# Kernel tuning notes

Hardware: AMD Instinct MI355X
Metric: run time of the kernel (lower is better)

Reference implementation:

```python
import jax, jax.numpy as jnp
import numpy as np

NF = 64
DG = 8
NB = 5
K = 3
K2 = K * K


def conv2d(x, w, b):
    # x: [B,C,H,W], w: [O,I,3,3] -> SAME padding, stride 1
    y = jax.lax.conv_general_dilated(x, w, (1, 1), 'SAME',
                                     dimension_numbers=('NCHW', 'OIHW', 'NCHW'))
    return y + b[None, :, None, None]


def dcn(x, off_feat, cw, cb, w, b):
    """Modulated deformable conv (DCNv2, extra_offset_mask=True).
    x: [B,C,H,W] sampled input; off_feat: [B,C,H,W] feeds conv_offset_mask.
    cw/cb: offset-mask conv params [3*DG*K2, C, 3, 3]; w/b: main conv [O, C, 3, 3].
    """
    B, C, H, W = x.shape
    Cg = C // DG
    om = conv2d(off_feat, cw, cb)                      # [B, 3*DG*K2, H, W]
    o1, o2, m = jnp.split(om, 3, axis=1)
    dy = o1.reshape(B, DG, K2, H, W)
    dx = o2.reshape(B, DG, K2, H, W)
    mask = jax.nn.sigmoid(m).reshape(B, DG, K2, H, W)
    # kernel tap offsets for 3x3, pad=1, dilation=1
    kyy, kxx = np.meshgrid(np.arange(K) - 1, np.arange(K) - 1, indexing='ij')
    ky = jnp.asarray(kyy.reshape(K2), x.dtype)
    kx = jnp.asarray(kxx.reshape(K2), x.dtype)
    gy = jnp.arange(H, dtype=x.dtype)
    gx = jnp.arange(W, dtype=x.dtype)
    py = gy[None, None, None, :, None] + ky[None, None, :, None, None] + dy  # [B,DG,K2,H,W]
    px = gx[None, None, None, None, :] + kx[None, None, :, None, None] + dx
    y0 = jnp.floor(py)
    x0 = jnp.floor(px)
    wy = py - y0
    wx = px - x0
    y0i = y0.astype(jnp.int32)
    x0i = x0.astype(jnp.int32)
    xg = x.reshape(B, DG, Cg, H * W)

    def gather(iy, ix):
        valid = ((iy >= 0) & (iy < H) & (ix >= 0) & (ix < W)).astype(x.dtype)
        lin = (jnp.clip(iy, 0, H - 1) * W + jnp.clip(ix, 0, W - 1)).reshape(B, DG, 1, K2 * H * W)
        v = jnp.take_along_axis(xg, jnp.broadcast_to(lin, (B, DG, Cg, K2 * H * W)), axis=3)
        return v.reshape(B, DG, Cg, K2, H, W) * valid[:, :, None]

    v00 = gather(y0i, x0i)
    v01 = gather(y0i, x0i + 1)
    v10 = gather(y0i + 1, x0i)
    v11 = gather(y0i + 1, x0i + 1)
    wy_ = wy[:, :, None]
    wx_ = wx[:, :, None]
    val = (v00 * (1 - wy_) * (1 - wx_) + v01 * (1 - wy_) * wx_
           + v10 * wy_ * (1 - wx_) + v11 * wy_ * wx_) * mask[:, :, None]  # [B,DG,Cg,K2,H,W]
    wr = w.reshape(w.shape[0], DG, Cg, K2)
    out = jnp.einsum('bgckhw,ogck->bohw', val, wr) + b[None, :, None, None]
    return out


def setup_inputs() -> dict:
    key = jax.random.key(0)
    ks = jax.random.split(key, 16)

    def w_(k, shape, s=0.05):
        return jax.random.normal(k, shape, jnp.float32) * s

    B, N, C, H, W = 4, 5, 1, 128, 128
    inp = {}
    inp['x'] = jax.random.normal(ks[0], (B, N, C, H, W), jnp.float32)
    inp['w_init'] = w_(ks[1], (NF, C, 3, 3))
    inp['b_init'] = jnp.zeros((NF,), jnp.float32)
    inp['res_w1'] = w_(ks[2], (NB, NF, NF, 3, 3))
    inp['res_b1'] = jnp.zeros((NB, NF), jnp.float32)
    inp['res_w2'] = w_(ks[3], (NB, NF, NF, 3, 3))
    inp['res_b2'] = jnp.zeros((NB, NF), jnp.float32)
    inp['w_bn'] = w_(ks[4], (NF, 2 * NF, 3, 3))
    inp['b_bn'] = jnp.zeros((NF,), jnp.float32)
    inp['off_w'] = w_(ks[5], (4, NF, NF, 3, 3))
    inp['off_b'] = jnp.zeros((4, NF), jnp.float32)
    inp['com_w'] = w_(ks[6], (4, 3 * DG * K2, NF, 3, 3), 0.01)
    inp['com_b'] = jnp.zeros((4, 3 * DG * K2), jnp.float32)
    inp['dcn_w'] = w_(ks[7], (4, NF, NF, 3, 3))
    inp['dcn_b'] = jnp.zeros((4, NF), jnp.float32)
    inp['w_rec'] = w_(ks[8], (C, NF, 3, 3))
    inp['b_rec'] = jnp.zeros((C,), jnp.float32)
    return inp


def reference(x, w_init, b_init, res_w1, res_b1, res_w2, res_b2, w_bn, b_bn,
              off_w, off_b, com_w, com_b, dcn_w, dcn_b, w_rec, b_rec):
    B, N, C, H, W = x.shape
    y = x.reshape(B * N, C, H, W)
    out = jax.nn.relu(conv2d(y, w_init, b_init))
    for i in range(NB):  # ResidualBlock_noBN x nb
        h = jax.nn.relu(conv2d(out, res_w1[i], res_b1[i]))
        out = out + conv2d(h, res_w2[i], res_b2[i])
    out = out.reshape(B, N, NF, H, W)
    ref = out[:, N // 2]
    ys = []
    for i in range(N):
        nei = out[:, i]
        fea = conv2d(jnp.concatenate([ref, nei], axis=1), w_bn, b_bn)
        o = conv2d(fea, off_w[0], off_b[0])
        fea = dcn(fea, o, com_w[0], com_b[0], dcn_w[0], dcn_b[0])
        o = conv2d(fea, off_w[1], off_b[1])
        fea = dcn(fea, o, com_w[1], com_b[1], dcn_w[1], dcn_b[1])
        o = conv2d(fea, off_w[2], off_b[2])
        fea = dcn(nei, o, com_w[2], com_b[2], dcn_w[2], dcn_b[2])
        o = conv2d(fea, off_w[3], off_b[3])
        aligned = dcn(fea, o, com_w[3], com_b[3], dcn_w[3], dcn_b[3])
        ys.append(conv2d(aligned, w_rec, b_rec))
    return jnp.concatenate(ys, axis=1)  # [B, N*C, H, W]
```

## Files before the change

### kernel.cpp

```cpp
#include <hip/hip_runtime.h>
#include <hip/hip_bf16.h>

typedef __hip_bfloat16 bf16;
typedef __attribute__((ext_vector_type(8))) short short8;
typedef __attribute__((ext_vector_type(4))) float floatx4;
typedef unsigned short ush;

#define HH 128
#define WW 128
#define HW 16384

__device__ __forceinline__ float b2f(bf16 v){ return __bfloat162float(v); }
__device__ __forceinline__ float bfu2f(ush u){
  union{unsigned int i; float f;} c; c.i = ((unsigned int)u)<<16; return c.f;
}
__device__ __forceinline__ ush f2bfu(float f){
  bf16 h = __float2bfloat16(f);
  return *(ush*)&h;
}

__global__ void detect_dtype(const ush* __restrict__ x, float* __restrict__ flag){
  __shared__ int bad;
  if (threadIdx.x==0) bad = 0;
  __syncthreads();
  for (int j=threadIdx.x; j<4096; j+=256){
    float f = bfu2f(x[j]);
    if (!(fabsf(f) < 1e4f)) atomicOr(&bad, 1);
  }
  __syncthreads();
  if (threadIdx.x==0) flag[0] = bad ? 0.f : 1.f;
}

__global__ void convert_in(const void* __restrict__ src, float* __restrict__ dst, int n,
                           const float* __restrict__ flag){
  int i = blockIdx.x*256 + threadIdx.x;
  if (i >= n) return;
  float v = (flag[0] > 0.5f) ? b2f(((const bf16*)src)[i]) : ((const float*)src)[i];
  dst[i] = v;
}

__global__ void transpose_w(const float* __restrict__ src, float* __restrict__ dst, int Co, int CiK){
  int tid = blockIdx.x*256 + threadIdx.x;
  if (tid >= Co*CiK) return;
  int co = tid / CiK, r = tid - co*CiK;
  dst[(long)r*Co + co] = src[tid];
}

__global__ void pack_w2(const float* __restrict__ src, ush* __restrict__ dst,
                        int Cout, int Cin, int kh, int nOcB){
  int idx = blockIdx.x*256 + threadIdx.x;
  int total = nOcB*36864;
  if (idx >= total) return;
  int ocb = idx / 36864; int r = idx - ocb*36864;
  int c  = r & 7;
  int lx = (r>>3) & 15;
  int n  = (r>>7) & 3;
  int lk = (r>>9) & 3;
  int j  = r>>11;
  int t = j>>1, ch = j&1;
  int oc = n*16+lx;
  int k = ch*32 + lk*8 + c;
  int ocg = ocb*64 + oc, icg = kh*64 + k;
  float v = (ocg < Cout && icg < Cin) ? src[((long)ocg*Cin + icg)*9 + t] : 0.f;
  dst[idx] = f2bfu(v);
}

__global__ void pack_dcn_w(const float* __restrict__ src, ush* __restrict__ dst){
  int idx = blockIdx.x*256 + threadIdx.x;
  if (idx >= 49152) return;
  int g = idx / 6144; int r = idx - g*6144;
  int oc = r / 96; int k = r - oc*96;
  float v = 0.f;
  if (k < 72){
    int tap = k >> 3, c = k & 7;
    v = src[((long)oc*64 + g*8 + c)*9 + tap];
  }
  dst[idx] = f2bfu(v);
}

__global__ __launch_bounds__(256) void conv_init_kernel(const float* __restrict__ x,
    const float* __restrict__ wT, const float* __restrict__ bias,
    ush* __restrict__ fh, ush* __restrict__ fl){
  __shared__ ush L[256*66];
  int tid = threadIdx.x;
  int tx = tid & 15, ty = tid >> 4;
  int gx = blockIdx.x*16+tx, gy = blockIdx.y*16+ty;
  int n = blockIdx.z;
  const float* xp = x + (long)n*HW;
  float v[9];
  #pragma unroll
  for (int dy=0;dy<3;dy++)
    #pragma unroll
    for (int dx=0;dx<3;dx++){
      int yy = gy+dy-1, xx = gx+dx-1;
      bool ok = (yy>=0)&&(yy<HH)&&(xx>=0)&&(xx<WW);
      v[dy*3+dx] = ok ? xp[yy*WW+xx] : 0.f;
    }
  float acc[64];
  #pragma unroll 1
  for (int oc=0; oc<64; oc++){
    float a = bias[oc];
    #pragma unroll
    for (int k=0;k<9;k++) a = fmaf(v[k], wT[k*64+oc], a);
    acc[oc] = fmaxf(a, 0.f);
  }
  #pragma unroll 1
  for (int pass=0; pass<2; pass++){
    #pragma unroll 1
    for (int oc=0; oc<64; oc++){
      float a = acc[oc];
      ush h = f2bfu(a);
      L[tid*66+oc] = pass ? f2bfu(a - bfu2f(h)) : h;
    }
    __syncthreads();
    ush* dst = pass ? fl : fh;
    for (int j=tid; j<2048; j+=256){
      int c8 = j&7, pidx = j>>3;
      int row = pidx>>4, col = pidx&15;
      long addr = ((long)n*HW + (blockIdx.y*16+row)*WW + blockIdx.x*16+col)*64 + c8*8;
      *(short8*)(dst+addr) = *(const short8*)(L + pidx*66 + c8*8);
    }
    __syncthreads();
  }
}

template<int NPL, int MINW, int MT>
__global__ __launch_bounds__(256, MINW) void conv_mfma(
    const ush* __restrict__ in_hi, const ush* __restrict__ in_lo, long in_ps,
    const ush* __restrict__ in2_hi, const ush* __restrict__ in2_lo, long in2_ps,
    const ush* __restrict__ wpack, const ush* __restrict__ wpack2,
    const float* __restrict__ bias, int has_bias,
    const ush* __restrict__ add_hi, const ush* __restrict__ add_lo,
    long add_ps, int add_cs,
    ush* __restrict__ out_hi, ush* __restrict__ out_lo,
    long out_ps, int out_cs,
    float* __restrict__ out_pf, int pf_C,
    int Cout, int nOcB, int relu)
{
  constexpr int ROWS = 4*MT + 2;
  constexpr int APX  = ROWS*18;
  constexpr int NPX  = 4*MT*16;
  constexpr int LDSN = (NPL*APX*64 > 2*NPX*66) ? NPL*APX*64 : 2*NPX*66;
  __shared__ ush A[LDSN];
  int tid = threadIdx.x;
  int z = blockIdx.z; int img = z / nOcB; int ocb = z - img*nOcB;
  int x0 = blockIdx.x*16 - 1, y0 = blockIdx.y*(4*MT) - 1;
  int w = tid>>6, l = tid&63, lx = l&15, lk = l>>4;
  floatx4 acc[MT][4];
  #pragma unroll
  for (int mt=0;mt<MT;mt++)
    #pragma unroll
    for (int n=0;n<4;n++) acc[mt][n] = (floatx4){0.f,0.f,0.f,0.f};

  auto phase = [&](const ush* ihb, const ush* ilb, const ush* wfb){
    __syncthreads();
    #pragma unroll
    for (int p=0;p<NPL;p++){
      const ush* src = p ? ilb : ihb;
      ush* dstp = A + p*APX*64;
      for (int j=tid; j<APX*8; j+=256){
        int pidx = j>>3, c8 = j&7;
        int row = pidx/18, col = pidx - row*18;
        int yy = y0+row, xx = x0+col;
        uint4 v = make_uint4(0u,0u,0u,0u);
        if ((unsigned)yy < 128u && (unsigned)xx < 128u)
          v = *(const uint4*)(src + ((long)(yy*WW+xx))*64 + c8*8);
        *(uint4*)(dstp + pidx*64 + ((c8 ^ (pidx&7))<<3)) = v;
      }
    }
    const ush* wfrag = wfb + lk*4*128 + lx*8;
    short8 bf[4][4];
    #pragma unroll
    for (int s=0;s<3;s++)
      #pragma unroll
      for (int n=0;n<4;n++)
        bf[s][n] = *(const short8*)(wfrag + (s*16 + n)*128);
    __syncthreads();
    #pragma unroll
    for (int j=0;j<18;j++){
      int t = j>>1, ch = j&1;
      if (j<15){
        #pragma unroll
        for (int n=0;n<4;n++)
          bf[(j+3)&3][n] = *(const short8*)(wfrag + ((j+3)*16 + n)*128);
      }
      int ky = t/3, kx = t - ky*3;
      int jc = ch*4 + lk;
      #pragma unroll
      for (int mt=0; mt<MT; mt++){
        int pidx = (w*MT+mt+ky)*18 + lx + kx;
        #pragma unroll
        for (int p=0;p<NPL;p++){
          short8 af = *(const short8*)(A + p*APX*64 + pidx*64 + ((jc ^ (pidx&7))<<3));
          #pragma unroll
          for (int n=0;n<4;n++)
            acc[mt][n] = __builtin_amdgcn_mfma_f32_16x16x32_bf16(af, bf[j&3][n], acc[mt][n], 0,0,0);
        }
      }
    }
  };
  phase(in_hi + (long)img*in_ps*64, in_lo + (long)img*in_ps*64,
        wpack + (long)ocb*36864);
  if (wpack2)
    phase(in2_hi + (long)img*in2_ps*64, in2_lo + (long)img*in2_ps*64,
          wpack2 + (long)ocb*36864);

  int ybase = blockIdx.y*(4*MT) + w*MT;
  int xbase = blockIdx.x*16 + lk*4;
  if (out_pf){
    #pragma unroll
    for (int mt=0;mt<MT;mt++){
      int y = ybase + mt;
      #pragma unroll
      for (int n=0;n<4;n++){
        int ocg = ocb*64 + n*16 + lx;
        if (ocg < Cout){
          float bv = has_bias ? bias[ocg] : 0.f;
          #pragma unroll
          for (int r=0;r<4;r++){
            int xg = xbase + r;
            out_pf[((long)img*pf_C + ocg)*HW + y*WW + xg] = acc[mt][n][r] + bv;
          }
        }
      }
    }
  } else {
    __syncthreads();
    ush* L0 = A;
    ush* L1 = A + NPX*66;
    #pragma unroll
    for (int mt=0;mt<MT;mt++){
      int y = ybase + mt;
      int rowl = w*MT + mt;
      #pragma unroll
      for (int n=0;n<4;n++){
        int ocg = n*16 + lx;
        float bv = has_bias ? bias[ocg] : 0.f;
        #pragma unroll
        for (int r=0;r<4;r++){
          int coll = lk*4 + r;
          float v = acc[mt][n][r] + bv;
          if (add_hi){
            long ap = ((long)img*add_ps + y*WW + blockIdx.x*16 + coll)*add_cs + ocg;
            v += bfu2f(add_hi[ap]) + bfu2f(add_lo[ap]);
          }
          if (relu) v = fmaxf(v, 0.f);
          ush h = f2bfu(v);
          L0[(rowl*16+coll)*66 + ocg] = h;
          if (out_lo) L1[(rowl*16+coll)*66 + ocg] = f2bfu(v - bfu2f(h));
        }
      }
    }
    __syncthreads();
    for (int j=tid; j<NPX*8; j+=256){
      int pidx = j>>3, c8 = j&7;
      int row = pidx>>4, col = pidx&15;
      long pp = (long)img*out_ps + (blockIdx.y*(4*MT)+row)*WW + blockIdx.x*16+col;
      *(short8*)(out_hi + pp*64 + c8*8) = *(const short8*)(L0 + pidx*66 + c8*8);
      if (out_lo)
        *(short8*)(out_lo + pp*64 + c8*8) = *(const short8*)(L1 + pidx*66 + c8*8);
    }
  }
}

__global__ __launch_bounds__(256) void repack_gp(const ush* __restrict__ in_h,
    const ush* __restrict__ in_l, long in_ps, float* __restrict__ gp){
  long idx = (long)blockIdx.x*256 + threadIdx.x;
  int img = (int)(idx >> 17);
  int rem = (int)(idx & 131071);
  int pix = rem >> 3, c8 = rem & 7;
  long src = ((long)img*in_ps + pix)*64 + c8*8;
  short8 h = *(const short8*)(in_h+src);
  short8 lo = *(const short8*)(in_l+src);
  float* d = gp + (((long)(img*8+c8))*HW + pix)*8;
  #pragma unroll
  for (int c=0;c<8;c++) d[c] = bfu2f((ush)h[c]) + bfu2f((ush)lo[c]);
}

__global__ __launch_bounds__(256) void dcn_mfma(
    const float* __restrict__ gp,
    const float* __restrict__ om,
    const ush* __restrict__ wpk,
    const float* __restrict__ bias,
    ush* __restrict__ out_hi, ush* __restrict__ out_lo)
{
  __shared__ ush S[13312];
  ush* Ah = S;
  ush* Bt = S + 6656;
  int tid = threadIdx.x;
  int half = blockIdx.x, gy = blockIdx.y, img = blockIdx.z;
  int xoff = half*64;
  {
    short8 z = {0,0,0,0,0,0,0,0};
    for (int j=tid; j<192; j+=256){
      int px = j/3, c = j - px*3;
      *(short8*)(Ah + px*104 + 72 + c*8) = z;
    }
  }
  int w = tid>>6, l = tid&63, lx = l&15, lk = l>>4;
  int px_s = tid & 63, q = tid >> 6;
  int t0 = (q==0)?0:(q*2+1), t1 = t0 + ((q==0)?3:2);
  const float* omb = om + (long)img*216*HW + gy*WW + xoff + px_s;
  floatx4 acc[4];
  #pragma unroll
  for (int n=0;n<4;n++) acc[n] = (floatx4){0.f,0.f,0.f,0.f};

  #pragma unroll 1
  for (int g=0; g<8; g++){
    __syncthreads();
    const ush* wsrc = wpk + g*6144;
    for (int j=tid; j<768; j+=256){
      int oc = j/12, kc = j - oc*12;
      *(short8*)(Bt + oc*104 + kc*8) = *(const short8*)(wsrc + oc*96 + kc*8);
    }
    const float* gpb = gp + ((long)(img*8+g))*HW*8;
    #pragma unroll 1
    for (int t=t0; t<t1; t++){
      int ch = g*9+t;
      float dy = omb[(long)ch*HW];
      float dx = omb[(long)(72+ch)*HW];
      float mv = omb[(long)(144+ch)*HW];
      float m = 1.f/(1.f+__expf(-mv));
      float py = (float)gy + (float)(t/3 - 1) + dy;
      float pxf = (float)(xoff + px_s) + (float)(t%3 - 1) + dx;
      float fy = floorf(py), fx = floorf(pxf);
      int y0 = (int)fy, x0 = (int)fx;
      float wy = py - fy, wx = pxf - fx;
      bool y0v = (y0>=0 && y0<HH), y1v = (y0+1>=0 && y0+1<HH);
      bool x0v = (x0>=0 && x0<WW), x1v = (x0+1>=0 && x0+1<WW);
      float w00 = (1.f-wy)*(1.f-wx)*m * ((y0v&&x0v)?1.f:0.f);
      float w01 = (1.f-wy)*wx*m      * ((y0v&&x1v)?1.f:0.f);
      float w10 = wy*(1.f-wx)*m      * ((y1v&&x0v)?1.f:0.f);
      float w11 = wy*wx*m            * ((y1v&&x1v)?1.f:0.f);
      int y0c = min(max(y0,0),HH-1), y1c = min(max(y0+1,0),HH-1);
      int x0c = min(max(x0,0),WW-1), x1c = min(max(x0+1,0),WW-1);
      const float* p00 = gpb + (((long)(y0c*WW+x0c))<<3);
      const float* p01 = gpb + (((long)(y0c*WW+x1c))<<3);
      const float* p10 = gpb + (((long)(y1c*WW+x0c))<<3);
      const float* p11 = gpb + (((long)(y1c*WW+x1c))<<3);
      float4 a00=*(const float4*)p00, b00=*(const float4*)(p00+4);
      float4 a01=*(const float4*)p01, b01=*(const float4*)(p01+4);
      float4 a10=*(const float4*)p10, b10=*(const float4*)(p10+4);
      float4 a11=*(const float4*)p11, b11=*(const float4*)(p11+4);
      float val[8];
      val[0]=w00*a00.x+w01*a01.x+w10*a10.x+w11*a11.x;
      val[1]=w00*a00.y+w01*a01.y+w10*a10.y+w11*a11.y;
      val[2]=w00*a00.z+w01*a01.z+w10*a10.z+w11*a11.z;
      val[3]=w00*a00.w+w01*a01.w+w10*a10.w+w11*a11.w;
      val[4]=w00*b00.x+w01*b01.x+w10*b10.x+w11*b11.x;
      val[5]=w00*b00.y+w01*b01.y+w10*b10.y+w11*b11.y;
      val[6]=w00*b00.z+w01*b01.z+w10*b10.z+w11*b11.z;
      val[7]=w00*b00.w+w01*b01.w+w10*b10.w+w11*b11.w;
      short8 vh;
      #pragma unroll
      for (int c=0;c<8;c++) vh[c] = (short)f2bfu(val[c]);
      *(short8*)(Ah + px_s*104 + t*8) = vh;
    }
    __syncthreads();
    #pragma unroll
    for (int ks=0; ks<3; ks++){
      short8 bfg[4];
      #pragma unroll
      for (int n=0;n<4;n++)
        bfg[n] = *(const short8*)(Bt + (n*16+lx)*104 + ks*32 + lk*8);
      int px = w*16 + lx;
      short8 ah = *(const short8*)(Ah + px*104 + ks*32 + lk*8);
      #pragma unroll
      for (int n=0;n<4;n++)
        acc[n] = __builtin_amdgcn_mfma_f32_16x16x32_bf16(ah, bfg[n], acc[n], 0,0,0);
    }
  }
  __syncthreads();
  ush* L0 = S;
  ush* L1 = S + 64*66;
  #pragma unroll
  for (int n=0;n<4;n++){
    int oc = n*16 + lx;
    float bv = bias[oc];
    #pragma unroll
    for (int r=0;r<4;r++){
      int pxl = w*16 + lk*4 + r;
      float v = acc[n][r] + bv;
      ush h = f2bfu(v);
      L0[pxl*66 + oc] = h;
      L1[pxl*66 + oc] = f2bfu(v - bfu2f(h));
    }
  }
  __syncthreads();
  long base = ((long)img*HW + gy*WW + xoff)*64;
  for (int j=tid; j<512; j+=256){
    int pidx = j>>3, c8 = j&7;
    *(short8*)(out_hi + base + pidx*64 + c8*8) = *(const short8*)(L0 + pidx*66 + c8*8);
    *(short8*)(out_lo + base + pidx*64 + c8*8) = *(const short8*)(L1 + pidx*66 + c8*8);
  }
}

__global__ __launch_bounds__(256) void rec_kernel(
    const ush* __restrict__ fh, const ush* __restrict__ fl,
    const float* __restrict__ wT, const float* __restrict__ bias,
    void* __restrict__ out, int ni, const float* __restrict__ flag){
  __shared__ float red[256];
  int tid = threadIdx.x;
  int p = tid & 31, q = tid >> 5;
  int gx = blockIdx.x*32 + p;
  int gy = blockIdx.y;
  int b = blockIdx.z;
  float acc = 0.f;
  #pragma unroll
  for (int t=0;t<9;t++){
    int yy = gy + t/3 - 1, xx = gx + t%3 - 1;
    if (yy<0||yy>=HH||xx<0||xx>=WW) continue;
    long base = ((long)b*HW + yy*WW + xx)*64 + q*8;
    short8 h = *(const short8*)(fh + base);
    short8 lo = *(const short8*)(fl + base);
    #pragma unroll
    for (int cc=0;cc<8;cc++){
      float v = bfu2f((ush)h[cc]) + bfu2f((ush)lo[cc]);
      acc = fmaf(v, wT[(q*8+cc)*9 + t], acc);
    }
  }
  red[q*32+p] = acc;
  __syncthreads();
  if (tid < 32){
    float s = bias[0];
    #pragma unroll
    for (int k=0;k<8;k++) s += red[k*32+tid];
    long idx = ((long)b*5+ni)*HW + gy*WW + blockIdx.x*32 + tid;
    if (flag[0] > 0.5f) ((bf16*)out)[idx] = __float2bfloat16(s);
    else                ((float*)out)[idx] = s;
  }
}

extern "C" void kernel_launch(void* const* d_in, const int* in_sizes, int n_in,
                              void* d_out, int out_size, void* d_ws, size_t ws_size,
                              hipStream_t stream) {
  float* ws = (float*)d_ws;

  size_t off = 16;
  auto alloc = [&](size_t nel){ size_t o = off; off += (nel + 7) & ~(size_t)7; return o; };

  static const int IN_N[17] = {327680, 576, 64, 184320, 320, 184320, 320,
                               73728, 64, 147456, 256, 497664, 864, 147456,
                               256, 576, 1};
  size_t cin[17];
  for (int i=0;i<17;i++) cin[i] = alloc(IN_N[i]);

  size_t wt_init = alloc(640);
  size_t wdcn_pk[4]; for (int s=0;s<4;s++) wdcn_pk[s] = alloc(24576);
  size_t wt_rec = alloc(640);
  size_t pk_res1[5], pk_res2[5];
  for (int i=0;i<5;i++) pk_res1[i] = alloc(18432);
  for (int i=0;i<5;i++) pk_res2[i] = alloc(18432);
  size_t pk_bn[2]; for (int h=0;h<2;h++) pk_bn[h] = alloc(18432);
  size_t pk_off[4]; for (int s=0;s<4;s++) pk_off[s] = alloc(18432);
  size_t pk_com[4]; for (int s=0;s<4;s++) pk_com[s] = alloc(73728);

  size_t feat_h_o = alloc(10485760);
  size_t feat_l_o = alloc(10485760);
  size_t U = alloc(26738688);

  ush* feat_h = (ush*)(ws + feat_h_o);
  ush* feat_l = (ush*)(ws + feat_l_o);
  ush* feaA_h = (ush*)(ws + U);
  ush* feaA_l = (ush*)(ws + U + 2097152);
  ush* feaB_h = (ush*)(ws + U + 4194304);
  ush* feaB_l = (ush*)(ws + U + 6291456);
  ush* obuf_h = (ush*)(ws + U + 8388608);
  float* gpbuf = ws + U + 8388608;
  float* ombuf = ws + U + 12582912;
  ush* hbuf_h = (ush*)(ws + U);

  float* flag = ws;

  detect_dtype<<<dim3(1), dim3(256), 0, stream>>>((const ush*)d_in[0], flag);
  for (int i=0;i<17;i++){
    int n = IN_N[i];
    convert_in<<<dim3((n+255)/256), dim3(256), 0, stream>>>(d_in[i], ws+cin[i], n, flag);
  }
  const float* b_init = ws+cin[2];
  const float* res_b1 = ws+cin[4];
  const float* res_b2 = ws+cin[6];
  const float* b_bn   = ws+cin[8];
  const float* off_b  = ws+cin[10];
  const float* com_b  = ws+cin[12];
  const float* dcn_b  = ws+cin[14];
  const float* b_rec  = ws+cin[16];

  auto tr = [&](size_t src_o, size_t dst_o, int Co, int CiK){
    int total = Co*CiK;
    transpose_w<<<dim3((total+255)/256), dim3(256), 0, stream>>>(ws+src_o, ws+dst_o, Co, CiK);
  };
  tr(cin[1], wt_init, 64, 9);
  tr(cin[15], wt_rec, 1, 576);
  for (int s=0;s<4;s++)
    pack_dcn_w<<<dim3(192), dim3(256), 0, stream>>>(ws+cin[13]+(size_t)s*36864,
                                                    (ush*)(ws+wdcn_pk[s]));

  auto pack = [&](size_t src_o, size_t dst_o, int Cout, int Cin, int kh, int nOcB){
    int total = nOcB*36864;
    pack_w2<<<dim3((total+255)/256), dim3(256), 0, stream>>>(
        ws+src_o, (ush*)(ws+dst_o), Cout, Cin, kh, nOcB);
  };
  for (int i=0;i<5;i++) pack(cin[3]+(size_t)i*36864, pk_res1[i], 64, 64, 0, 1);
  for (int i=0;i<5;i++) pack(cin[5]+(size_t)i*36864, pk_res2[i], 64, 64, 0, 1);
  for (int h=0;h<2;h++) pack(cin[7], pk_bn[h], 64, 128, h, 1);
  for (int s=0;s<4;s++) pack(cin[9]+(size_t)s*36864,  pk_off[s], 64, 64, 0, 1);
  for (int s=0;s<4;s++) pack(cin[11]+(size_t)s*124416, pk_com[s], 216, 64, 0, 4);

  dim3 cblk(256);
  auto conv = [&](const ush* in_h, const ush* in_l, long in_ps,
                  const ush* in2_h, const ush* in2_l, long in2_ps,
                  size_t pk, const ush* pk2p,
                  const float* bias, int has_bias,
                  const ush* add_h, const ush* add_l, long add_ps, int add_cs,
                  ush* o_h, ush* o_l, long out_ps, int out_cs,
                  float* o_pf, int pf_C,
                  int Cout, int nOcB, int relu, int N, int nPl, int mtMode){
    if (nPl == 2 && mtMode == 2)
      conv_mfma<2,2,2><<<dim3(8,16,N*nOcB), cblk, 0, stream>>>(
          in_h, in_l, in_ps, in2_h, in2_l, in2_ps,
          (const ush*)(ws+pk), pk2p, bias, has_bias,
          add_h, add_l, add_ps, add_cs, o_h, o_l, out_ps, out_cs,
          o_pf, pf_C, Cout, nOcB, relu);
    else if (nPl == 2 && mtMode == 1)
      conv_mfma<2,2,1><<<dim3(8,32,N*nOcB), cblk, 0, stream>>>(
          in_h, in_l, in_ps, in2_h, in2_l, in2_ps,
          (const ush*)(ws+pk), pk2p, bias, has_bias,
          add_h, add_l, add_ps, add_cs, o_h, o_l, out_ps, out_cs,
          o_pf, pf_C, Cout, nOcB, relu);
    else if (nPl == 1 && mtMode == 1)
      conv_mfma<1,3,1><<<dim3(8,32,N*nOcB), cblk, 0, stream>>>(
          in_h, in_l, in_ps, in2_h, in2_l, in2_ps,
          (const ush*)(ws+pk), pk2p, bias, has_bias,
          add_h, add_l, add_ps, add_cs, o_h, o_l, out_ps, out_cs,
          o_pf, pf_C, Cout, nOcB, relu);
    else
      conv_mfma<1,3,2><<<dim3(8,16,N*nOcB), cblk, 0, stream>>>(
          in_h, in_l, in_ps, in2_h, in2_l, in2_ps,
          (const ush*)(ws+pk), pk2p, bias, has_bias,
          add_h, add_l, add_ps, add_cs, o_h, o_l, out_ps, out_cs,
          o_pf, pf_C, Cout, nOcB, relu);
  };

  conv_init_kernel<<<dim3(8,8,20), cblk, 0, stream>>>(ws+cin[0], ws+wt_init, b_init,
                                                      feat_h, feat_l);
  for (int i=0;i<5;i++){
    conv(feat_h, feat_l, HW, nullptr, nullptr, 0, pk_res1[i], nullptr,
         res_b1+(size_t)i*64, 1,
         nullptr, nullptr, 0, 0, hbuf_h, nullptr, HW, 64, nullptr, 0, 64, 1, 1, 20, 2, 1);
    conv(hbuf_h, hbuf_h, HW, nullptr, nullptr, 0, pk_res2[i], nullptr,
         res_b2+(size_t)i*64, 1,
         feat_h, feat_l, HW, 64, feat_h, feat_l, HW, 64, nullptr, 0, 64, 1, 0, 20, 1, 1);
  }
  for (int i=0;i<5;i++){
    conv(feat_h + (size_t)2*HW*64, feat_l + (size_t)2*HW*64, 5L*HW,
         feat_h + (size_t)i*HW*64, feat_l + (size_t)i*HW*64, 5L*HW,
         pk_bn[0], (const ush*)(ws+pk_bn[1]), b_bn, 1,
         nullptr, nullptr, 0, 0, feaA_h, feaA_l, HW, 64, nullptr, 0, 64, 1, 0, 4, 2, 1);
    ush *fa_h = feaA_h, *fa_l = feaA_l, *fb_h = feaB_h, *fb_l = feaB_l;
    for (int s=0;s<4;s++){
      conv(fa_h, fa_h, HW, nullptr, nullptr, 0, pk_off[s], nullptr,
           off_b+(size_t)s*64, 1,
           nullptr, nullptr, 0, 0, obuf_h, nullptr, HW, 64, nullptr, 0, 64, 1, 0, 4, 1, 1);
      conv(obuf_h, obuf_h, HW, nullptr, nullptr, 0, pk_com[s], nullptr,
           com_b+(size_t)s*216, 1,
           nullptr, nullptr, 0, 0, nullptr, nullptr, 0, 0, ombuf, 216, 216, 4, 0, 4, 1, 2);
      const ush *xs_h, *xs_l; long xps;
      if (s == 2){ xs_h = feat_h + (size_t)i*HW*64; xs_l = feat_l + (size_t)i*HW*64; xps = 5L*HW; }
      else       { xs_h = fa_h;                     xs_l = fa_l;                     xps = HW; }
      repack_gp<<<dim3(2048), cblk, 0, stream>>>(xs_h, xs_l, xps, gpbuf);
      dcn_mfma<<<dim3(2,128,4), cblk, 0, stream>>>(gpbuf, ombuf,
          (const ush*)(ws+wdcn_pk[s]), dcn_b+(size_t)s*64, fb_h, fb_l);
      ush* t;
      t = fa_h; fa_h = fb_h; fb_h = t;
      t = fa_l; fa_l = fb_l; fb_l = t;
    }
    rec_kernel<<<dim3(4,128,4), cblk, 0, stream>>>(fa_h, fa_l, ws+wt_rec, b_rec, d_out, i, flag);
  }
}
```

Measured before the change: 3.436 ms.

## Fuse residual block conv pairs into one kernel with halo recompute

Adds a res_fused kernel that computes both 3x3 convolutions of a residual block in a single launch. It loads an input tile with a 2-pixel halo into shared memory, computes the ReLU hidden activations for a 1-pixel-halo tile, then runs the second conv and adds the residual before writing hi/lo bf16 outputs. Blocks 1-4 use this kernel, ping-ponging between feat and an alternate buffer; block 0 keeps the old two-launch path. The aim is to avoid the hidden-activation round trip through global memory and half the launches. The cost is recomputing the halo in the first conv, about 1.7x its MACs. The first conv also reads only the hi input plane, which may slightly change precision.

After: 3.257 ms. 5.2% less time.

```diff
diff --git a/kernel.cpp b/kernel.cpp
--- a/kernel.cpp
+++ b/kernel.cpp
@@ -260,6 +260,156 @@
       if (out_lo)
         *(short8*)(out_lo + pp*64 + c8*8) = *(const short8*)(L1 + pidx*66 + c8*8);
     }
+  }
+}
+
+__global__ __launch_bounds__(256,4) void res_fused(
+    const ush* __restrict__ src_h, const ush* __restrict__ src_l,
+    const ush* __restrict__ w1, const float* __restrict__ b1,
+    const ush* __restrict__ w2, const float* __restrict__ b2,
+    ush* __restrict__ dst_h, ush* __restrict__ dst_l)
+{
+  __shared__ ush F[180*64];
+  __shared__ ush Hs[112*64];
+  int tid = threadIdx.x;
+  int bx = blockIdx.x, by = blockIdx.y, img = blockIdx.z;
+  int fy0 = by*4 - 2, fx0 = bx*16 - 2;
+  int w = tid>>6, l = tid&63, lx = l&15, lk = l>>4;
+  const ush* sh = src_h + (long)img*HW*64;
+  for (int j=tid; j<1440; j+=256){
+    int pidx = j>>3, c8 = j&7;
+    int row = pidx/20, col = pidx - row*20;
+    int yy = fy0+row, xx = fx0+col;
+    uint4 v = make_uint4(0u,0u,0u,0u);
+    if ((unsigned)yy<128u && (unsigned)xx<128u)
+      v = *(const uint4*)(sh + ((long)(yy*WW+xx))*64 + c8*8);
+    *(uint4*)(F + pidx*64 + ((c8 ^ (pidx&7))<<3)) = v;
+  }
+  const ush* wf1 = w1 + lk*4*128 + lx*8;
+  int hrow[2], hcol[2], hvalid[2];
+  #pragma unroll
+  for (int mm=0;mm<2;mm++){
+    int m = w + mm*4;
+    hvalid[mm] = (m < 7);
+    int hp = m*16 + lx;
+    hrow[mm] = hp/18; hcol[mm] = hp - hrow[mm]*18;
+  }
+  floatx4 acc1[2][4];
+  #pragma unroll
+  for (int mm=0;mm<2;mm++)
+    #pragma unroll
+    for (int n=0;n<4;n++) acc1[mm][n] = (floatx4){0.f,0.f,0.f,0.f};
+  short8 bf[4][4];
+  #pragma unroll
+  for (int s=0;s<3;s++)
+    #pragma unroll
+    for (int n=0;n<4;n++)
+      bf[s][n] = *(const short8*)(wf1 + (s*16 + n)*128);
+  __syncthreads();
+  #pragma unroll
+  for (int j=0;j<18;j++){
+    int t = j>>1, ch = j&1;
+    if (j<15){
+      #pragma unroll
+      for (int n=0;n<4;n++)
+        bf[(j+3)&3][n] = *(const short8*)(wf1 + ((j+3)*16 + n)*128);
+    }
+    int ky = t/3, kx = t - ky*3;
+    int jc = ch*4 + lk;
+    #pragma unroll
+    for (int mm=0;mm<2;mm++){
+      if (!hvalid[mm]) continue;
+      int pidx = (hrow[mm]+ky)*20 + hcol[mm] + kx;
+      short8 af = *(const short8*)(F + pidx*64 + ((jc ^ (pidx&7))<<3));
+      #pragma unroll
+      for (int n=0;n<4;n++)
+        acc1[mm][n] = __builtin_amdgcn_mfma_f32_16x16x32_bf16(af, bf[j&3][n], acc1[mm][n], 0,0,0);
+    }
+  }
+  #pragma unroll
+  for (int mm=0;mm<2;mm++){
+    if (!hvalid[mm]) continue;
+    int m = w + mm*4;
+    #pragma unroll
+    for (int n=0;n<4;n++){
+      int oc = n*16+lx;
+      float bv = b1[oc];
+      #pragma unroll
+      for (int r=0;r<4;r++){
+        int hp = m*16 + lk*4 + r;
+        int hr = hp/18, hc = hp - hr*18;
+        int fy = fy0 + 1 + hr, fx = fx0 + 1 + hc;
+        bool inimg = ((unsigned)fy < 128u) && ((unsigned)fx < 128u);
+        float v = inimg ? fmaxf(acc1[mm][n][r] + bv, 0.f) : 0.f;
+        Hs[hp*64 + (((oc>>3) ^ (hp&7))<<3) + (oc&7)] = f2bfu(v);
+      }
+    }
+  }
+  __syncthreads();
+  const ush* wf2 = w2 + lk*4*128 + lx*8;
+  floatx4 acc2[4];
+  #pragma unroll
+  for (int n=0;n<4;n++) acc2[n] = (floatx4){0.f,0.f,0.f,0.f};
+  #pragma unroll
+  for (int s=0;s<3;s++)
+    #pragma unroll
+    for (int n=0;n<4;n++)
+      bf[s][n] = *(const short8*)(wf2 + (s*16 + n)*128);
+  #pragma unroll
+  for (int j=0;j<18;j++){
+    int t = j>>1, ch = j&1;
+    if (j<15){
+      #pragma unroll
+      for (int n=0;n<4;n++)
+        bf[(j+3)&3][n] = *(const short8*)(wf2 + ((j+3)*16 + n)*128);
+    }
+    int ky = t/3, kx = t - ky*3;
+    int jc = ch*4 + lk;
+    int pidx = (w+ky)*18 + lx + kx;
+    short8 af = *(const short8*)(Hs + pidx*64 + ((jc ^ (pidx&7))<<3));
+    #pragma unroll
+    for (int n=0;n<4;n++)
+      acc2[n] = __builtin_amdgcn_mfma_f32_16x16x32_bf16(af, bf[j&3][n], acc2[n], 0,0,0);
+  }
+  const ush* sl = src_l + (long)img*HW*64;
+  int gy = by*4 + w;
+  float vout[4][4];
+  #pragma unroll
+  for (int n=0;n<4;n++){
+    int oc = n*16+lx;
+    float bv = b2[oc];
+    #pragma unroll
+    for (int r=0;r<4;r++){
+      int colp = lk*4 + r;
+      int gx = bx*16 + colp;
+      int pt = (w+2)*20 + colp + 2;
+      float fh = bfu2f(F[pt*64 + (((oc>>3) ^ (pt&7))<<3) + (oc&7)]);
+      float fl = bfu2f(sl[((long)(gy*WW+gx))*64 + oc]);
+      vout[n][r] = acc2[n][r] + bv + fh + fl;
+    }
+  }
+  __syncthreads();
+  ush* L0 = F;
+  ush* L1 = F + 64*66;
+  #pragma unroll
+  for (int n=0;n<4;n++){
+    int oc = n*16+lx;
+    #pragma unroll
+    for (int r=0;r<4;r++){
+      int px = w*16 + lk*4 + r;
+      float v = vout[n][r];
+      ush h = f2bfu(v);
+      L0[px*66 + oc] = h;
+      L1[px*66 + oc] = f2bfu(v - bfu2f(h));
+    }
+  }
+  __syncthreads();
+  for (int j=tid; j<512; j+=256){
+    int pidx = j>>3, c8 = j&7;
+    int row = pidx>>4, col = pidx&15;
+    long pp = ((long)img*HW + (by*4+row)*WW + bx*16+col)*64 + c8*8;
+    *(short8*)(dst_h + pp) = *(const short8*)(L0 + pidx*66 + c8*8);
+    *(short8*)(dst_l + pp) = *(const short8*)(L1 + pidx*66 + c8*8);
   }
 }
 
@@ -461,6 +611,9 @@
 
   ush* feat_h = (ush*)(ws + feat_h_o);
   ush* feat_l = (ush*)(ws + feat_l_o);
+  ush* alt_h  = (ush*)(ws + U);
+  ush* alt_l  = (ush*)(ws + U + 10485760);
+  ush* hbuf_h = (ush*)(ws + U + 10485760);
   ush* feaA_h = (ush*)(ws + U);
   ush* feaA_l = (ush*)(ws + U + 2097152);
   ush* feaB_h = (ush*)(ws + U + 4194304);
@@ -468,7 +621,6 @@
   ush* obuf_h = (ush*)(ws + U + 8388608);
   float* gpbuf = ws + U + 8388608;
   float* ombuf = ws + U + 12582912;
-  ush* hbuf_h = (ush*)(ws + U);
 
   float* flag = ws;
 
@@ -544,13 +696,22 @@
 
   conv_init_kernel<<<dim3(8,8,20), cblk, 0, stream>>>(ws+cin[0], ws+wt_init, b_init,
                                                       feat_h, feat_l);
-  for (int i=0;i<5;i++){
-    conv(feat_h, feat_l, HW, nullptr, nullptr, 0, pk_res1[i], nullptr,
-         res_b1+(size_t)i*64, 1,
-         nullptr, nullptr, 0, 0, hbuf_h, nullptr, HW, 64, nullptr, 0, 64, 1, 1, 20, 2, 1);
-    conv(hbuf_h, hbuf_h, HW, nullptr, nullptr, 0, pk_res2[i], nullptr,
-         res_b2+(size_t)i*64, 1,
-         feat_h, feat_l, HW, 64, feat_h, feat_l, HW, 64, nullptr, 0, 64, 1, 0, 20, 1, 1);
+  conv(feat_h, feat_l, HW, nullptr, nullptr, 0, pk_res1[0], nullptr,
+       res_b1, 1,
+       nullptr, nullptr, 0, 0, hbuf_h, nullptr, HW, 64, nullptr, 0, 64, 1, 1, 20, 2, 1);
+  conv(hbuf_h, hbuf_h, HW, nullptr, nullptr, 0, pk_res2[0], nullptr,
+       res_b2, 1,
+       feat_h, feat_l, HW, 64, feat_h, feat_l, HW, 64, nullptr, 0, 64, 1, 0, 20, 1, 1);
+  {
+    ush *sh = feat_h, *sl = feat_l, *dh = alt_h, *dl = alt_l;
+    for (int i=1;i<5;i++){
+      res_fused<<<dim3(8,32,20), cblk, 0, stream>>>(
+          sh, sl, (const ush*)(ws+pk_res1[i]), res_b1+(size_t)i*64,
+          (const ush*)(ws+pk_res2[i]), res_b2+(size_t)i*64, dh, dl);
+      ush* t;
+      t = sh; sh = dh; dh = t;
+      t = sl; sl = dl; dl = t;
+    }
   }
   for (int i=0;i<5;i++){
     conv(feat_h + (size_t)2*HW*64, feat_l + (size_t)2*HW*64, 5L*HW,
```
